# Performance work log

Hardware: AMD Instinct MI355X
Metric: run time of the kernel (lower is better)

The kernel has to match this reference:

```python
import jax, jax.numpy as jnp
import numpy as np


def setup_inputs() -> dict:
    key = jax.random.key(0)
    k1, k2 = jax.random.split(key)
    x1 = jax.random.normal(k1, (8192, 64), dtype=jnp.float32)
    x2 = jax.random.normal(k2, (8192, 64), dtype=jnp.float32)
    return {"x1": x1, "x2": x2}


def reference(x1, x2):
    # squared Euclidean distance: ||a-b||^2 = ||a||^2 + ||b||^2 - 2 a.b
    sq1 = jnp.sum(x1 * x1, axis=-1, keepdims=True)        # [N, 1]
    sq2 = jnp.sum(x2 * x2, axis=-1, keepdims=True).T      # [1, M]
    cross = jnp.einsum('nd,md->nm', x1, x2)               # [N, M] GEMM
    d2 = sq1 + sq2 - 2.0 * cross
    # clamp tiny negatives from floating-point cancellation (cdist>=0)
    return jnp.maximum(d2, 0.0)
```

## Files before the change

### kernel.cpp

```cpp
#include <hip/hip_runtime.h>


#define TILE 128
#define KDIM 64
#define LDS_STRIDE 132

__global__ __launch_bounds__(256, 2)
void sqeuclid_kernel(const float* __restrict__ x1,
                     const float* __restrict__ x2,
                     float* __restrict__ out,
                     int N, int M) {
    __shared__ float a_s[KDIM][LDS_STRIDE];
    __shared__ float b_s[KDIM][LDS_STRIDE];
    __shared__ float sq1_s[TILE];
    __shared__ float sq2_s[TILE];

    const int t = threadIdx.x;
    const int block_row = blockIdx.y * TILE;
    const int block_col = blockIdx.x * TILE;

    {
        const int kv = t & 15;
        #pragma unroll
        for (int it = 0; it < 2; ++it) {
            const int rg = (t >> 4) + it * 16;
            const int r  = rg * 4;
            const float4 a0 = *(const float4*)(x1 + (size_t)(block_row + r + 0) * KDIM + kv * 4);
            const float4 a1 = *(const float4*)(x1 + (size_t)(block_row + r + 1) * KDIM + kv * 4);
            const float4 a2 = *(const float4*)(x1 + (size_t)(block_row + r + 2) * KDIM + kv * 4);
            const float4 a3 = *(const float4*)(x1 + (size_t)(block_row + r + 3) * KDIM + kv * 4);
            *(float4*)&a_s[kv * 4 + 0][r] = make_float4(a0.x, a1.x, a2.x, a3.x);
            *(float4*)&a_s[kv * 4 + 1][r] = make_float4(a0.y, a1.y, a2.y, a3.y);
            *(float4*)&a_s[kv * 4 + 2][r] = make_float4(a0.z, a1.z, a2.z, a3.z);
            *(float4*)&a_s[kv * 4 + 3][r] = make_float4(a0.w, a1.w, a2.w, a3.w);

            const float4 b0 = *(const float4*)(x2 + (size_t)(block_col + r + 0) * KDIM + kv * 4);
            const float4 b1 = *(const float4*)(x2 + (size_t)(block_col + r + 1) * KDIM + kv * 4);
            const float4 b2 = *(const float4*)(x2 + (size_t)(block_col + r + 2) * KDIM + kv * 4);
            const float4 b3 = *(const float4*)(x2 + (size_t)(block_col + r + 3) * KDIM + kv * 4);
            *(float4*)&b_s[kv * 4 + 0][r] = make_float4(b0.x, b1.x, b2.x, b3.x);
            *(float4*)&b_s[kv * 4 + 1][r] = make_float4(b0.y, b1.y, b2.y, b3.y);
            *(float4*)&b_s[kv * 4 + 2][r] = make_float4(b0.z, b1.z, b2.z, b3.z);
            *(float4*)&b_s[kv * 4 + 3][r] = make_float4(b0.w, b1.w, b2.w, b3.w);
        }
    }
    __syncthreads();

    if (t < TILE) {
        float s = 0.f;
        #pragma unroll 8
        for (int k = 0; k < KDIM; ++k) { const float v = a_s[k][t]; s = fmaf(v, v, s); }
        sq1_s[t] = s;
    } else {
        const int m = t - TILE;
        float s = 0.f;
        #pragma unroll 8
        for (int k = 0; k < KDIM; ++k) { const float v = b_s[k][m]; s = fmaf(v, v, s); }
        sq2_s[m] = s;
    }
    __syncthreads();

    const int wave = t >> 6;
    const int lane = t & 63;
    const int row0 = (wave >> 1) * 64 + (lane >> 3) * 8;
    const int col0 = (wave & 1) * 64 + (lane & 7) * 8;

    float acc[8][8];
    #pragma unroll
    for (int i = 0; i < 8; ++i)
        #pragma unroll
        for (int j = 0; j < 8; ++j) acc[i][j] = 0.f;

    for (int k = 0; k < KDIM; ++k) {
        const float4 aA = *(const float4*)&a_s[k][row0];
        const float4 aB = *(const float4*)&a_s[k][row0 + 4];
        const float4 bA = *(const float4*)&b_s[k][col0];
        const float4 bB = *(const float4*)&b_s[k][col0 + 4];
        const float ar[8] = {aA.x, aA.y, aA.z, aA.w, aB.x, aB.y, aB.z, aB.w};
        const float br[8] = {bA.x, bA.y, bA.z, bA.w, bB.x, bB.y, bB.z, bB.w};
        #pragma unroll
        for (int i = 0; i < 8; ++i)
            #pragma unroll
            for (int j = 0; j < 8; ++j)
                acc[i][j] = fmaf(ar[i], br[j], acc[i][j]);
    }

    #pragma unroll
    for (int i = 0; i < 8; ++i) {
        const size_t gr = (size_t)(block_row + row0 + i) * M + block_col + col0;
        const float s1 = sq1_s[row0 + i];
        float4 o0, o1;
        o0.x = fmaxf(fmaf(-2.f, acc[i][0], s1 + sq2_s[col0 + 0]), 0.f);
        o0.y = fmaxf(fmaf(-2.f, acc[i][1], s1 + sq2_s[col0 + 1]), 0.f);
        o0.z = fmaxf(fmaf(-2.f, acc[i][2], s1 + sq2_s[col0 + 2]), 0.f);
        o0.w = fmaxf(fmaf(-2.f, acc[i][3], s1 + sq2_s[col0 + 3]), 0.f);
        o1.x = fmaxf(fmaf(-2.f, acc[i][4], s1 + sq2_s[col0 + 4]), 0.f);
        o1.y = fmaxf(fmaf(-2.f, acc[i][5], s1 + sq2_s[col0 + 5]), 0.f);
        o1.z = fmaxf(fmaf(-2.f, acc[i][6], s1 + sq2_s[col0 + 6]), 0.f);
        o1.w = fmaxf(fmaf(-2.f, acc[i][7], s1 + sq2_s[col0 + 7]), 0.f);
        *(float4*)(out + gr)     = o0;
        *(float4*)(out + gr + 4) = o1;
    }
}

extern "C" void kernel_launch(void* const* d_in, const int* in_sizes, int n_in,
                              void* d_out, int out_size, void* d_ws, size_t ws_size,
                              hipStream_t stream) {
    const float* x1 = (const float*)d_in[0];
    const float* x2 = (const float*)d_in[1];
    float* out = (float*)d_out;
    const int N = in_sizes[0] / KDIM;
    const int M = in_sizes[1] / KDIM;

    dim3 grid(M / TILE, N / TILE);
    dim3 block(256);
    sqeuclid_kernel<<<grid, block, 0, stream>>>(x1, x2, out, N, M);
}
```

Measured before the change: 333.0 us.

## Use bf16 MFMA for cross term with fused norm computation during load

Replaces the FP32 scalar-FMA outer-product GEMM with 16x16x32 bf16 MFMA instructions. Inputs are converted to bf16 while being staged into LDS in a row-major layout, and the fp32 row norms are accumulated during the same load pass, which removes one barrier and the separate norm loop. Output stores become per-element, coalesced across 16 lanes. Rounding the dot products to bf16 reduces accuracy, and cancellation in ||a||^2+||b||^2-2ab may push errors past tolerance.

```diff
diff --git a/kernel.cpp b/kernel.cpp
--- a/kernel.cpp
+++ b/kernel.cpp
@@ -1,17 +1,25 @@
 #include <hip/hip_runtime.h>
 
 
+typedef __bf16 bf16x8 __attribute__((ext_vector_type(8)));
+typedef float floatx4 __attribute__((ext_vector_type(4)));
+typedef unsigned short ushort8 __attribute__((ext_vector_type(8)));
+
 #define TILE 128
-#define KDIM 64
-#define LDS_STRIDE 132
+#define KD 64
+#define LDSS 72
 
-__global__ __launch_bounds__(256, 2)
-void sqeuclid_kernel(const float* __restrict__ x1,
-                     const float* __restrict__ x2,
-                     float* __restrict__ out,
-                     int N, int M) {
-    __shared__ float a_s[KDIM][LDS_STRIDE];
-    __shared__ float b_s[KDIM][LDS_STRIDE];
+__device__ __forceinline__ unsigned short f2bf(float x) {
+    union { float f; unsigned int u; } v; v.f = x;
+    return (unsigned short)((v.u + 0x7FFFu + ((v.u >> 16) & 1u)) >> 16);
+}
+
+__global__ void sqeuclid_mfma(const float* __restrict__ x1,
+                              const float* __restrict__ x2,
+                              float* __restrict__ out,
+                              int M) {
+    __shared__ unsigned short a_s[TILE][LDSS];
+    __shared__ unsigned short b_s[TILE][LDSS];
     __shared__ float sq1_s[TILE];
     __shared__ float sq2_s[TILE];
 
@@ -20,86 +28,71 @@
     const int block_col = blockIdx.x * TILE;
 
     {
-        const int kv = t & 15;
+        const int r = t & 127;
+        const float* src = (t < TILE) ? (x1 + (size_t)(block_row + r) * KD)
+                                      : (x2 + (size_t)(block_col + r) * KD);
+        unsigned short* dst = (t < TILE) ? a_s[r] : b_s[r];
+        float nrm = 0.f;
         #pragma unroll
-        for (int it = 0; it < 2; ++it) {
-            const int rg = (t >> 4) + it * 16;
-            const int r  = rg * 4;
-            const float4 a0 = *(const float4*)(x1 + (size_t)(block_row + r + 0) * KDIM + kv * 4);
-            const float4 a1 = *(const float4*)(x1 + (size_t)(block_row + r + 1) * KDIM + kv * 4);
-            const float4 a2 = *(const float4*)(x1 + (size_t)(block_row + r + 2) * KDIM + kv * 4);
-            const float4 a3 = *(const float4*)(x1 + (size_t)(block_row + r + 3) * KDIM + kv * 4);
-            *(float4*)&a_s[kv * 4 + 0][r] = make_float4(a0.x, a1.x, a2.x, a3.x);
-            *(float4*)&a_s[kv * 4 + 1][r] = make_float4(a0.y, a1.y, a2.y, a3.y);
-            *(float4*)&a_s[kv * 4 + 2][r] = make_float4(a0.z, a1.z, a2.z, a3.z);
-            *(float4*)&a_s[kv * 4 + 3][r] = make_float4(a0.w, a1.w, a2.w, a3.w);
-
-            const float4 b0 = *(const float4*)(x2 + (size_t)(block_col + r + 0) * KDIM + kv * 4);
-            const float4 b1 = *(const float4*)(x2 + (size_t)(block_col + r + 1) * KDIM + kv * 4);
-            const float4 b2 = *(const float4*)(x2 + (size_t)(block_col + r + 2) * KDIM + kv * 4);
-            const float4 b3 = *(const float4*)(x2 + (size_t)(block_col + r + 3) * KDIM + kv * 4);
-            *(float4*)&b_s[kv * 4 + 0][r] = make_float4(b0.x, b1.x, b2.x, b3.x);
-            *(float4*)&b_s[kv * 4 + 1][r] = make_float4(b0.y, b1.y, b2.y, b3.y);
-            *(float4*)&b_s[kv * 4 + 2][r] = make_float4(b0.z, b1.z, b2.z, b3.z);
-            *(float4*)&b_s[kv * 4 + 3][r] = make_float4(b0.w, b1.w, b2.w, b3.w);
+        for (int i = 0; i < 8; ++i) {
+            const float4 f0 = ((const float4*)src)[2 * i];
+            const float4 f1 = ((const float4*)src)[2 * i + 1];
+            nrm = fmaf(f0.x, f0.x, nrm); nrm = fmaf(f0.y, f0.y, nrm);
+            nrm = fmaf(f0.z, f0.z, nrm); nrm = fmaf(f0.w, f0.w, nrm);
+            nrm = fmaf(f1.x, f1.x, nrm); nrm = fmaf(f1.y, f1.y, nrm);
+            nrm = fmaf(f1.z, f1.z, nrm); nrm = fmaf(f1.w, f1.w, nrm);
+            ushort8 pk;
+            pk[0] = f2bf(f0.x); pk[1] = f2bf(f0.y); pk[2] = f2bf(f0.z); pk[3] = f2bf(f0.w);
+            pk[4] = f2bf(f1.x); pk[5] = f2bf(f1.y); pk[6] = f2bf(f1.z); pk[7] = f2bf(f1.w);
+            *(ushort8*)&dst[i * 8] = pk;
         }
+        if (t < TILE) sq1_s[r] = nrm; else sq2_s[r] = nrm;
     }
     __syncthreads();
 
-    if (t < TILE) {
-        float s = 0.f;
-        #pragma unroll 8
-        for (int k = 0; k < KDIM; ++k) { const float v = a_s[k][t]; s = fmaf(v, v, s); }
-        sq1_s[t] = s;
-    } else {
-        const int m = t - TILE;
-        float s = 0.f;
-        #pragma unroll 8
-        for (int k = 0; k < KDIM; ++k) { const float v = b_s[k][m]; s = fmaf(v, v, s); }
-        sq2_s[m] = s;
-    }
-    __syncthreads();
+    const int wave = t >> 6, lane = t & 63;
+    const int wr = (wave >> 1) * 64;
+    const int wc = (wave & 1) * 64;
+    const int lm = lane & 15, lq = lane >> 4;
 
-    const int wave = t >> 6;
-    const int lane = t & 63;
-    const int row0 = (wave >> 1) * 64 + (lane >> 3) * 8;
-    const int col0 = (wave & 1) * 64 + (lane & 7) * 8;
+    floatx4 acc[4][4];
+    #pragma unroll
+    for (int i = 0; i < 4; ++i)
+        #pragma unroll
+        for (int j = 0; j < 4; ++j)
+            acc[i][j] = (floatx4){0.f, 0.f, 0.f, 0.f};
 
-    float acc[8][8];
     #pragma unroll
-    for (int i = 0; i < 8; ++i)
+    for (int ks = 0; ks < 2; ++ks) {
+        const int koff = ks * 32 + lq * 8;
+        bf16x8 afr[4], bfr[4];
         #pragma unroll
-        for (int j = 0; j < 8; ++j) acc[i][j] = 0.f;
-
-    for (int k = 0; k < KDIM; ++k) {
-        const float4 aA = *(const float4*)&a_s[k][row0];
-        const float4 aB = *(const float4*)&a_s[k][row0 + 4];
-        const float4 bA = *(const float4*)&b_s[k][col0];
-        const float4 bB = *(const float4*)&b_s[k][col0 + 4];
-        const float ar[8] = {aA.x, aA.y, aA.z, aA.w, aB.x, aB.y, aB.z, aB.w};
-        const float br[8] = {bA.x, bA.y, bA.z, bA.w, bB.x, bB.y, bB.z, bB.w};
+        for (int i = 0; i < 4; ++i) {
+            afr[i] = *(const bf16x8*)&a_s[wr + i * 16 + lm][koff];
+            bfr[i] = *(const bf16x8*)&b_s[wc + i * 16 + lm][koff];
+        }
         #pragma unroll
-        for (int i = 0; i < 8; ++i)
+        for (int i = 0; i < 4; ++i)
             #pragma unroll
-            for (int j = 0; j < 8; ++j)
-                acc[i][j] = fmaf(ar[i], br[j], acc[i][j]);
+            for (int j = 0; j < 4; ++j)
+                acc[i][j] = __builtin_amdgcn_mfma_f32_16x16x32_bf16(
+                    afr[i], bfr[j], acc[i][j], 0, 0, 0);
     }
 
     #pragma unroll
-    for (int i = 0; i < 8; ++i) {
-        const size_t gr = (size_t)(block_row + row0 + i) * M + block_col + col0;
-        const float s1 = sq1_s[row0 + i];
-        float4 o0, o1;
-        o0.x = fmaxf(fmaf(-2.f, acc[i][0], s1 + sq2_s[col0 + 0]), 0.f);
-        o0.y = fmaxf(fmaf(-2.f, acc[i][1], s1 + sq2_s[col0 + 1]), 0.f);
-        o0.z = fmaxf(fmaf(-2.f, acc[i][2], s1 + sq2_s[col0 + 2]), 0.f);
-        o0.w = fmaxf(fmaf(-2.f, acc[i][3], s1 + sq2_s[col0 + 3]), 0.f);
-        o1.x = fmaxf(fmaf(-2.f, acc[i][4], s1 + sq2_s[col0 + 4]), 0.f);
-        o1.y = fmaxf(fmaf(-2.f, acc[i][5], s1 + sq2_s[col0 + 5]), 0.f);
-        o1.z = fmaxf(fmaf(-2.f, acc[i][6], s1 + sq2_s[col0 + 6]), 0.f);
-        o1.w = fmaxf(fmaf(-2.f, acc[i][7], s1 + sq2_s[col0 + 7]), 0.f);
-        *(float4*)(out + gr)     = o0;
-        *(float4*)(out + gr + 4) = o1;
+    for (int i = 0; i < 4; ++i) {
+        #pragma unroll
+        for (int r = 0; r < 4; ++r) {
+            const int lrow = wr + i * 16 + lq * 4 + r;
+            const float s1 = sq1_s[lrow];
+            const size_t gbase = (size_t)(block_row + lrow) * M + block_col;
+            #pragma unroll
+            for (int j = 0; j < 4; ++j) {
+                const int lcol = wc + j * 16 + lm;
+                const float v = fmaf(-2.f, acc[i][j][r], s1 + sq2_s[lcol]);
+                out[gbase + lcol] = fmaxf(v, 0.f);
+            }
+        }
     }
 }
 
@@ -109,10 +102,10 @@
     const float* x1 = (const float*)d_in[0];
     const float* x2 = (const float*)d_in[1];
     float* out = (float*)d_out;
-    const int N = in_sizes[0] / KDIM;
-    const int M = in_sizes[1] / KDIM;
+    const int N = in_sizes[0] / KD;
+    const int M = in_sizes[1] / KD;
 
     dim3 grid(M / TILE, N / TILE);
     dim3 block(256);
-    sqeuclid_kernel<<<grid, block, 0, stream>>>(x1, x2, out, N, M);
+    sqeuclid_mfma<<<grid, block, 0, stream>>>(x1, x2, out, M);
 }
```

After: 278.1 us. 1.2x faster.
